# Optimization experiments

Measured on AMD Instinct MI355X. Metric: run time of the kernel, lower is better.

Reference implementation:

```python
import jax, jax.numpy as jnp
import numpy as np

N = 50000      # nodes
E = 800000     # edges (before self loops)
NF = 4         # node feature dim
EF = 4         # edge feature dim
EMB = 16       # joint embedding dim
HID = 64       # hidden dim
OUT = 128      # output dim
H = 4          # heads (layers 0,1); last layer has 1 head
NEG_SLOPE = 0.2


def setup_inputs() -> dict:
    key = jax.random.key(0)
    ks = jax.random.split(key, 20)
    in0 = NF + EMB  # 20

    def lin(k, o, i):
        return (jax.random.normal(k, (o, i), jnp.float32) * np.float32(1.0 / np.sqrt(i)))

    return {
        'x': jax.random.normal(ks[0], (N, NF), jnp.float32),
        'edge_index': jax.random.randint(ks[1], (2, E), 0, N, dtype=jnp.int32),
        'edge_attr': jax.random.normal(ks[2], (E, EF), jnp.float32),
        'joint_types': jax.random.randint(ks[3], (N,), 0, 17, dtype=jnp.int32),
        'emb_table': jax.random.normal(ks[4], (17, EMB), jnp.float32) * 0.1,
        'W0': lin(ks[5], H * HID, in0),
        'a_src0': jax.random.normal(ks[6], (H, HID), jnp.float32) * 0.1,
        'a_dst0': jax.random.normal(ks[7], (H, HID), jnp.float32) * 0.1,
        'We0': lin(ks[8], H, EF),
        'W1': lin(ks[9], H * HID, HID),
        'a_src1': jax.random.normal(ks[10], (H, HID), jnp.float32) * 0.1,
        'a_dst1': jax.random.normal(ks[11], (H, HID), jnp.float32) * 0.1,
        'We1': lin(ks[12], H, EF),
        'W2': lin(ks[13], 1 * OUT, HID),
        'a_src2': jax.random.normal(ks[14], (1, OUT), jnp.float32) * 0.1,
        'a_dst2': jax.random.normal(ks[15], (1, OUT), jnp.float32) * 0.1,
        'We2': lin(ks[16], 1, EF),
    }


def gat_layer(x, src, dst, eattr, W, a_src, a_dst, We, num_nodes):
    # x: [N, F_in]; W: [H*C, F_in]; a_src/a_dst: [H, C]; We: [H, EF]
    Hh, C = a_src.shape
    h = (x @ W.T).reshape(num_nodes, Hh, C)  # [N, H, C]
    # per-node attention scores, gathered per edge (same math as per-edge dot)
    s_i = jnp.einsum('nhc,hc->nh', h, a_src)  # applied to x_i = x[dst]
    s_j = jnp.einsum('nhc,hc->nh', h, a_dst)  # applied to x_j = x[src]
    alpha = s_i[dst] + s_j[src] + eattr @ We.T  # [Etot, H]
    alpha = jax.nn.leaky_relu(alpha, NEG_SLOPE)
    # faithful to torch.softmax(alpha, dim=0): GLOBAL softmax over all edges per head
    alpha = jax.nn.softmax(alpha, axis=0)
    msgs = h[src] * alpha[:, :, None]  # [Etot, H, C]
    out = jax.ops.segment_sum(msgs, dst, num_segments=num_nodes)  # aggr='add'
    return out.mean(axis=1)  # update(): mean over heads -> [N, C]


def reference(x, edge_index, edge_attr, joint_types, emb_table,
              W0, a_src0, a_dst0, We0,
              W1, a_src1, a_dst1, We1,
              W2, a_src2, a_dst2, We2):
    num_nodes = x.shape[0]
    # add self loops (edge_attr fill 0.0)
    loops = jnp.arange(num_nodes, dtype=edge_index.dtype)
    src = jnp.concatenate([edge_index[0], loops])
    dst = jnp.concatenate([edge_index[1], loops])
    eattr = jnp.concatenate([edge_attr, jnp.zeros((num_nodes, edge_attr.shape[1]), edge_attr.dtype)], axis=0)

    h = jnp.concatenate([x, emb_table[joint_types]], axis=-1)  # [N, 20]
    h = gat_layer(h, src, dst, eattr, W0, a_src0, a_dst0, We0, num_nodes)
    h = jax.nn.elu(h)  # dropout is identity in eval mode
    h = gat_layer(h, src, dst, eattr, W1, a_src1, a_dst1, We1, num_nodes)
    h = jax.nn.elu(h)
    h = gat_layer(h, src, dst, eattr, W2, a_src2, a_dst2, We2, num_nodes)
    return h  # [N, OUT]
```

## Files before the change

kernel.cpp:

```cpp
#include <hip/hip_runtime.h>
#include <math.h>

#define NN 50000
#define EE 800000
#define EEN (EE+NN)
#define STRIDE 64
#define NFEAT 4
#define EFEAT 4
#define EMBD 16
#define IN0 20
#define HIDD 64
#define OUTD 128

__device__ __forceinline__ unsigned short f2bf(float f){
  unsigned u = __float_as_uint(f);
  return (unsigned short)((u + 0x7FFFu + ((u>>16)&1u)) >> 16);
}
__device__ __forceinline__ float bfl(unsigned u){ return __uint_as_float(u<<16); }
__device__ __forceinline__ float bfh(unsigned u){ return __uint_as_float(u & 0xFFFF0000u); }

template<int V> struct ldt;
template<> struct ldt<4>{ using T = uint2; };
template<> struct ldt<2>{ using T = unsigned int; };

__global__ void k_init(int* fill){
  int i = blockIdx.x*blockDim.x + threadIdx.x;
  if (i < NN) fill[i]=0;
}

__global__ void k_scatter(const int* __restrict__ ei, int* fill,
                          int* __restrict__ col, int* __restrict__ epos){
  int idx = blockIdx.x*blockDim.x + threadIdx.x;
  if (idx < EE){
    int d = ei[EE+idx];
    int pos = atomicAdd(&fill[d],1);
    col[d*STRIDE + 1 + pos] = ei[idx];
    epos[idx] = d*STRIDE + 1 + pos;
  } else if (idx < EEN){
    int n = idx-EE;
    col[n*STRIDE] = n;
  }
}

template<int F_IN,int HH,int CC>
__device__ __forceinline__ void av_one(const float* W, const float* asrc,
                                       const float* adst, float* av, int tid){
  if (tid >= HH*F_IN) return;
  int h = tid / F_IN, f = tid % F_IN;
  float s1=0.f, s2=0.f;
  for (int c=0;c<CC;c++){
    float wv = W[(size_t)(h*CC+c)*F_IN+f];
    s1 += asrc[h*CC+c]*wv;
    s2 += adst[h*CC+c]*wv;
  }
  av[tid] = s1;
  av[HH*F_IN+tid] = s2;
}
__global__ void k_av3(const float* W0, const float* as0, const float* ad0, float* av0,
                      const float* W1, const float* as1, const float* ad1, float* av1,
                      const float* W2, const float* as2, const float* ad2, float* av2,
                      float* zred){
  int tid = threadIdx.x;
  if      (blockIdx.x==0){ av_one<IN0,4,64> (W0, as0, ad0, av0, tid); if (tid<24) zred[tid]=0.f; }
  else if (blockIdx.x==1) av_one<64,4,64>  (W1, as1, ad1, av1, tid);
  else                    av_one<64,1,128> (W2, as2, ad2, av2, tid);
}

template<int K,int NCOL,int HH,bool CONCAT>
__global__ __launch_bounds__(256)
void k_gemm(const float* __restrict__ xin, const int* __restrict__ jt,
            const float* __restrict__ emb, const float* __restrict__ W,
            const float* __restrict__ avp, unsigned short* __restrict__ hout,
            float* __restrict__ si, float* __restrict__ sj){
  constexpr int PITCH = 132;
  __shared__ float xT[K*PITCH];
  __shared__ float wT[K*PITCH];
  __shared__ float EMBL[CONCAT ? 17*EMBD : 1];
  int tid = threadIdx.x;
  int rbase = blockIdx.x*128, cbase = blockIdx.y*128;
  if (CONCAT){
    for (int i=tid; i<17*EMBD; i+=256) EMBL[i]=emb[i];
    __syncthreads();
    if (tid < 128){
      int row = tid;
      int gr = rbase+row; if (gr >= NN) gr = NN-1;
      float4 v = ((const float4*)xin)[gr];
      xT[0*PITCH+row]=v.x; xT[1*PITCH+row]=v.y;
      xT[2*PITCH+row]=v.z; xT[3*PITCH+row]=v.w;
      int j = jt[gr];
      #pragma unroll
      for (int k=0;k<EMBD;k++) xT[(NFEAT+k)*PITCH+row] = EMBL[j*EMBD+k];
    } else {
      int col = tid-128;
      const float4* wp = (const float4*)(W + (size_t)(cbase+col)*K);
      #pragma unroll
      for (int k4=0;k4<K/4;k4++){
        float4 v = wp[k4];
        wT[(4*k4+0)*PITCH+col]=v.x; wT[(4*k4+1)*PITCH+col]=v.y;
        wT[(4*k4+2)*PITCH+col]=v.z; wT[(4*k4+3)*PITCH+col]=v.w;
      }
    }
  } else {
    constexpr int K4 = K/4;
    for (int i=tid; i<128*K4; i+=256){
      int row = i/K4, k4 = i%K4;
      int gr = rbase+row; if (gr >= NN) gr = NN-1;
      float4 v = ((const float4*)xin)[(size_t)gr*K4 + k4];
      xT[(4*k4+0)*PITCH+row]=v.x; xT[(4*k4+1)*PITCH+row]=v.y;
      xT[(4*k4+2)*PITCH+row]=v.z; xT[(4*k4+3)*PITCH+row]=v.w;
    }
    for (int i=tid; i<128*K4; i+=256){
      int col = i/K4, k4 = i%K4;
      float4 v = ((const float4*)W)[(size_t)(cbase+col)*K4 + k4];
      wT[(4*k4+0)*PITCH+col]=v.x; wT[(4*k4+1)*PITCH+col]=v.y;
      wT[(4*k4+2)*PITCH+col]=v.z; wT[(4*k4+3)*PITCH+col]=v.w;
    }
  }
  __syncthreads();
  int lane = tid & 63, w = tid >> 6;
  int r0 = (w>>1)*64 + (lane&7)*8;
  int c0 = (w&1)*64 + (lane>>3)*8;
  float acc[8][8];
  #pragma unroll
  for (int i=0;i<8;i++)
    #pragma unroll
    for (int j=0;j<8;j++) acc[i][j]=0.f;
  #pragma unroll 4
  for (int k=0;k<K;k++){
    float a[8], b[8];
    *(float4*)&a[0] = *(const float4*)&xT[k*PITCH + r0];
    *(float4*)&a[4] = *(const float4*)&xT[k*PITCH + r0 + 4];
    *(float4*)&b[0] = *(const float4*)&wT[k*PITCH + c0];
    *(float4*)&b[4] = *(const float4*)&wT[k*PITCH + c0 + 4];
    #pragma unroll
    for (int i=0;i<8;i++)
      #pragma unroll
      for (int j=0;j<8;j++) acc[i][j] += a[i]*b[j];
  }
  if (blockIdx.y==0 && tid < 128){
    int row = tid, gr = rbase+row;
    if (gr < NN){
      #pragma unroll
      for (int h=0;h<HH;h++){
        float a=0.f, b=0.f;
        for (int k=0;k<K;k++){
          float xv = xT[k*PITCH+row];
          a += xv*avp[h*K+k];
          b += xv*avp[HH*K+h*K+k];
        }
        si[(size_t)gr*HH+h]=a;
        sj[(size_t)gr*HH+h]=b;
      }
    }
  }
  #pragma unroll
  for (int i=0;i<8;i++){
    int n = rbase + r0 + i;
    if (n < NN){
      uint4 o;
      o.x = (unsigned)f2bf(acc[i][0]) | ((unsigned)f2bf(acc[i][1])<<16);
      o.y = (unsigned)f2bf(acc[i][2]) | ((unsigned)f2bf(acc[i][3])<<16);
      o.z = (unsigned)f2bf(acc[i][4]) | ((unsigned)f2bf(acc[i][5])<<16);
      o.w = (unsigned)f2bf(acc[i][6]) | ((unsigned)f2bf(acc[i][7])<<16);
      *(uint4*)(hout + (size_t)n*NCOL + cbase + c0) = o;
    }
  }
}

template<int HH>
__global__ void k_edge(const int* __restrict__ ei, const float* __restrict__ eattr,
                       const float* __restrict__ We, const float* __restrict__ si,
                       const float* __restrict__ sj, const int* __restrict__ epos,
                       float* __restrict__ pp, float* __restrict__ zred){
  int idx = blockIdx.x*blockDim.x + threadIdx.x;
  float z[HH];
  #pragma unroll
  for (int h=0;h<HH;h++) z[h]=0.f;
  if (idx < EE){
    int s = ei[idx], d = ei[EE+idx];
    const float4 ea = ((const float4*)eattr)[idx];
    int pos = epos[idx];
    if (HH==4){
      float4 siv = ((const float4*)si)[d];
      float4 sjv = ((const float4*)sj)[s];
      float te[4] = {siv.x+sjv.x, siv.y+sjv.y, siv.z+sjv.z, siv.w+sjv.w};
      float pv[4];
      #pragma unroll
      for (int h=0;h<4;h++){
        float t = te[h] + ea.x*We[h*EFEAT+0] + ea.y*We[h*EFEAT+1]
                        + ea.z*We[h*EFEAT+2] + ea.w*We[h*EFEAT+3];
        t = (t>0.f)? t : 0.2f*t;
        float p = expf(t);
        z[h]=p; pv[h]=p;
      }
      ((float4*)pp)[pos] = make_float4(pv[0],pv[1],pv[2],pv[3]);
    } else {
      float t = si[d] + sj[s]
              + ea.x*We[0] + ea.y*We[1] + ea.z*We[2] + ea.w*We[3];
      t = (t>0.f)? t : 0.2f*t;
      float p = expf(t);
      z[0]=p;
      pp[pos] = p;
    }
  } else if (idx < EEN){
    int n = idx-EE;
    int pos = n*STRIDE;
    if (HH==4){
      float4 siv = ((const float4*)si)[n];
      float4 sjv = ((const float4*)sj)[n];
      float te[4] = {siv.x+sjv.x, siv.y+sjv.y, siv.z+sjv.z, siv.w+sjv.w};
      float pv[4];
      #pragma unroll
      for (int h=0;h<4;h++){
        float t = te[h];
        t = (t>0.f)? t : 0.2f*t;
        float p = expf(t);
        z[h]=p; pv[h]=p;
      }
      ((float4*)pp)[pos] = make_float4(pv[0],pv[1],pv[2],pv[3]);
    } else {
      float t = si[n]+sj[n];
      t = (t>0.f)? t : 0.2f*t;
      float p = expf(t);
      z[0]=p;
      pp[pos]=p;
    }
  }
  __shared__ float zs[4][HH];
  #pragma unroll
  for (int h=0;h<HH;h++){
    float v=z[h];
    #pragma unroll
    for (int off=32; off>0; off>>=1) v += __shfl_xor(v,off,64);
    if ((threadIdx.x&63)==0) zs[threadIdx.x>>6][h]=v;
  }
  __syncthreads();
  if (threadIdx.x < HH){
    float tot = zs[0][threadIdx.x]+zs[1][threadIdx.x]
              + zs[2][threadIdx.x]+zs[3][threadIdx.x];
    atomicAdd(&zred[threadIdx.x], tot);
  }
}

template<int HH,int CC,bool DO_ELU>
__global__ __launch_bounds__(256)
void k_agg(const unsigned short* __restrict__ hb, const float* __restrict__ pp,
           const float* __restrict__ zred, const int* __restrict__ fill,
           const int* __restrict__ col, float* __restrict__ outp){
  constexpr int HC = HH*CC;
  constexpr int V  = HC/64;
  using LT = typename ldt<V>::T;
  int wave = threadIdx.x>>6, lane = threadIdx.x&63;
  int n = blockIdx.x*4 + wave;
  int hd = (lane*V)/CC;
  float invZ = 1.0f/zred[hd];
  float acc[V];
  #pragma unroll
  for (int v=0;v<V;v++) acc[v]=0.f;
  auto mac = [&](float p, LT h){
    if constexpr (V==4){
      acc[0] += p*bfl(h.x); acc[1] += p*bfh(h.x);
      acc[2] += p*bfl(h.y); acc[3] += p*bfh(h.y);
    } else {
      acc[0] += p*bfl(h);   acc[1] += p*bfh(h);
    }
  };
  int beg = n*STRIDE, end = beg + 1 + fill[n];
  int i = beg;
  for (; i+8<=end; i+=8){
    int sr[8]; float p[8]; LT h[8];
    #pragma unroll
    for (int k=0;k<8;k++) sr[k]=col[i+k];
    #pragma unroll
    for (int k=0;k<8;k++)
      p[k] = (HH==4) ? pp[(size_t)(i+k)*4+hd] : pp[i+k];
    #pragma unroll
    for (int k=0;k<8;k++) h[k]=((const LT*)(hb + (size_t)sr[k]*HC))[lane];
    #pragma unroll
    for (int k=0;k<8;k++) mac(p[k], h[k]);
  }
  for (; i<end; i++){
    int sr = col[i];
    float p = (HH==4) ? pp[(size_t)i*4+hd] : pp[i];
    LT h = ((const LT*)(hb + (size_t)sr*HC))[lane];
    mac(p, h);
  }
  #pragma unroll
  for (int v=0;v<V;v++) acc[v] *= invZ;
  if (HH==4){
    #pragma unroll
    for (int off=16; off<64; off<<=1){
      #pragma unroll
      for (int v=0;v<V;v++) acc[v] += __shfl_xor(acc[v], off, 64);
    }
    if (lane < 16){
      float4 o;
      o.x=0.25f*acc[0]; o.y=0.25f*acc[1]; o.z=0.25f*acc[2]; o.w=0.25f*acc[3];
      if (DO_ELU){
        o.x = (o.x>0.f)? o.x : expm1f(o.x);
        o.y = (o.y>0.f)? o.y : expm1f(o.y);
        o.z = (o.z>0.f)? o.z : expm1f(o.z);
        o.w = (o.w>0.f)? o.w : expm1f(o.w);
      }
      ((float4*)outp)[(size_t)n*(CC/4)+lane] = o;
    }
  } else {
    float2 o; o.x=acc[0]; o.y=acc[1];
    if (DO_ELU){
      o.x = (o.x>0.f)? o.x : expm1f(o.x);
      o.y = (o.y>0.f)? o.y : expm1f(o.y);
    }
    ((float2*)outp)[(size_t)n*(CC/2)+lane] = o;
  }
}

extern "C" void kernel_launch(void* const* d_in, const int* in_sizes, int n_in,
                              void* d_out, int out_size, void* d_ws, size_t ws_size,
                              hipStream_t stream){
  const float* x    = (const float*)d_in[0];
  const int*   ei   = (const int*)d_in[1];
  const float* eatt = (const float*)d_in[2];
  const int*   jt   = (const int*)d_in[3];
  const float* emb  = (const float*)d_in[4];
  const float* W0   = (const float*)d_in[5];
  const float* as0  = (const float*)d_in[6];
  const float* ad0  = (const float*)d_in[7];
  const float* We0  = (const float*)d_in[8];
  const float* W1   = (const float*)d_in[9];
  const float* as1  = (const float*)d_in[10];
  const float* ad1  = (const float*)d_in[11];
  const float* We1  = (const float*)d_in[12];
  const float* W2   = (const float*)d_in[13];
  const float* as2  = (const float*)d_in[14];
  const float* ad2  = (const float*)d_in[15];
  const float* We2  = (const float*)d_in[16];
  float* out = (float*)d_out;

  char* p = (char*)d_ws;
  auto alloc = [&](size_t bytes)->char*{
    char* r = p; p += (bytes + 255) & ~(size_t)255; return r;
  };
  unsigned short* hbuf = (unsigned short*)alloc((size_t)NN*256*2);
  float* x1     = (float*)alloc((size_t)NN*64*4);
  float* x2     = (float*)alloc((size_t)NN*64*4);
  float* si     = (float*)alloc((size_t)NN*4*4);
  float* sj     = (float*)alloc((size_t)NN*4*4);
  float* pp     = (float*)alloc((size_t)NN*STRIDE*16);
  int*   fill   = (int*)alloc((size_t)NN*4);
  int*   col    = (int*)alloc((size_t)NN*STRIDE*4);
  int*   epos   = (int*)alloc((size_t)EE*4);
  float* av0    = (float*)alloc(512*4);
  float* av1    = (float*)alloc(512*4);
  float* av2    = (float*)alloc(512*4);
  float* zred   = (float*)alloc(3*8*4);

  k_init   <<<dim3((NN+255)/256),  256, 0, stream>>>(fill);
  k_scatter<<<dim3((EEN+255)/256), 256, 0, stream>>>(ei, fill, col, epos);
  k_av3    <<<dim3(3),             256, 0, stream>>>(W0,as0,ad0,av0, W1,as1,ad1,av1,
                                                     W2,as2,ad2,av2, zred);

  dim3 gg01((NN+127)/128, 2);
  dim3 gg2 ((NN+127)/128, 1);
  dim3 egrid((EEN+255)/256);
  dim3 agrid(NN/4);

  k_gemm<IN0,256,4,true> <<<gg01, 256, 0, stream>>>(x, jt, emb, W0, av0, hbuf, si, sj);
  k_edge<4>              <<<egrid,256, 0, stream>>>(ei, eatt, We0, si, sj, epos, pp, zred+0);
  k_agg<4,64,true>       <<<agrid,256, 0, stream>>>(hbuf, pp, zred+0, fill, col, x1);

  k_gemm<64,256,4,false> <<<gg01, 256, 0, stream>>>(x1, jt, emb, W1, av1, hbuf, si, sj);
  k_edge<4>              <<<egrid,256, 0, stream>>>(ei, eatt, We1, si, sj, epos, pp, zred+8);
  k_agg<4,64,true>       <<<agrid,256, 0, stream>>>(hbuf, pp, zred+8, fill, col, x2);

  k_gemm<64,128,1,false> <<<gg2,  256, 0, stream>>>(x2, jt, emb, W2, av2, hbuf, si, sj);
  k_edge<1>              <<<egrid,256, 0, stream>>>(ei, eatt, We2, si, sj, epos, pp, zred+16);
  k_agg<1,128,false>     <<<agrid,256, 0, stream>>>(hbuf, pp, zred+16, fill, col, out);
}
```

Before: 539.6 us.

## Reorder edge attributes into CSR slots and compute edge scores per destination node

The scatter pass now copies edge attributes into the padded CSR slot layout. The edge-score kernel then processes one destination node per wave, reading col and attributes contiguously and using the node's own si value. This removes the epos indirection, the random pp writes and the per-edge si gathers. In exchange the work per wave is capped at 64 lanes, so nodes with fewer edges leave lanes idle, and the padded attribute buffer is large.

```diff
diff --git a/kernel.cpp b/kernel.cpp
--- a/kernel.cpp
+++ b/kernel.cpp
@@ -28,14 +28,15 @@
   if (i < NN) fill[i]=0;
 }
 
-__global__ void k_scatter(const int* __restrict__ ei, int* fill,
-                          int* __restrict__ col, int* __restrict__ epos){
+__global__ void k_scatter(const int* __restrict__ ei, const float4* __restrict__ eattr,
+                          int* fill, int* __restrict__ col, float4* __restrict__ eacsr){
   int idx = blockIdx.x*blockDim.x + threadIdx.x;
   if (idx < EE){
     int d = ei[EE+idx];
     int pos = atomicAdd(&fill[d],1);
-    col[d*STRIDE + 1 + pos] = ei[idx];
-    epos[idx] = d*STRIDE + 1 + pos;
+    int slot = d*STRIDE + 1 + pos;
+    col[slot] = ei[idx];
+    eacsr[slot] = eattr[idx];
   } else if (idx < EEN){
     int n = idx-EE;
     col[n*STRIDE] = n;
@@ -168,20 +169,25 @@
 }
 
 template<int HH>
-__global__ void k_edge(const int* __restrict__ ei, const float* __restrict__ eattr,
-                       const float* __restrict__ We, const float* __restrict__ si,
-                       const float* __restrict__ sj, const int* __restrict__ epos,
-                       float* __restrict__ pp, float* __restrict__ zred){
-  int idx = blockIdx.x*blockDim.x + threadIdx.x;
+__global__ __launch_bounds__(256)
+void k_edge2(const int* __restrict__ col, const float4* __restrict__ eacsr,
+             const int* __restrict__ fill, const float* __restrict__ We,
+             const float* __restrict__ si, const float* __restrict__ sj,
+             float* __restrict__ pp, float* __restrict__ zred){
+  int wave = threadIdx.x>>6, lane = threadIdx.x&63;
+  int n = blockIdx.x*4 + wave;
+  int cnt = 1 + fill[n];
   float z[HH];
   #pragma unroll
   for (int h=0;h<HH;h++) z[h]=0.f;
-  if (idx < EE){
-    int s = ei[idx], d = ei[EE+idx];
-    const float4 ea = ((const float4*)eattr)[idx];
-    int pos = epos[idx];
+  if (lane < cnt){
+    int slot = n*STRIDE + lane;
+    int s = col[slot];
+    float4 ea;
+    if (lane==0){ ea = make_float4(0.f,0.f,0.f,0.f); }
+    else        { ea = eacsr[slot]; }
     if (HH==4){
-      float4 siv = ((const float4*)si)[d];
+      float4 siv = ((const float4*)si)[n];
       float4 sjv = ((const float4*)sj)[s];
       float te[4] = {siv.x+sjv.x, siv.y+sjv.y, siv.z+sjv.z, siv.w+sjv.w};
       float pv[4];
@@ -193,37 +199,14 @@
         float p = expf(t);
         z[h]=p; pv[h]=p;
       }
-      ((float4*)pp)[pos] = make_float4(pv[0],pv[1],pv[2],pv[3]);
+      ((float4*)pp)[slot] = make_float4(pv[0],pv[1],pv[2],pv[3]);
     } else {
-      float t = si[d] + sj[s]
+      float t = si[n] + sj[s]
               + ea.x*We[0] + ea.y*We[1] + ea.z*We[2] + ea.w*We[3];
       t = (t>0.f)? t : 0.2f*t;
       float p = expf(t);
       z[0]=p;
-      pp[pos] = p;
-    }
-  } else if (idx < EEN){
-    int n = idx-EE;
-    int pos = n*STRIDE;
-    if (HH==4){
-      float4 siv = ((const float4*)si)[n];
-      float4 sjv = ((const float4*)sj)[n];
-      float te[4] = {siv.x+sjv.x, siv.y+sjv.y, siv.z+sjv.z, siv.w+sjv.w};
-      float pv[4];
-      #pragma unroll
-      for (int h=0;h<4;h++){
-        float t = te[h];
-        t = (t>0.f)? t : 0.2f*t;
-        float p = expf(t);
-        z[h]=p; pv[h]=p;
-      }
-      ((float4*)pp)[pos] = make_float4(pv[0],pv[1],pv[2],pv[3]);
-    } else {
-      float t = si[n]+sj[n];
-      t = (t>0.f)? t : 0.2f*t;
-      float p = expf(t);
-      z[0]=p;
-      pp[pos]=p;
+      pp[slot] = p;
     }
   }
   __shared__ float zs[4][HH];
@@ -232,7 +215,7 @@
     float v=z[h];
     #pragma unroll
     for (int off=32; off>0; off>>=1) v += __shfl_xor(v,off,64);
-    if ((threadIdx.x&63)==0) zs[threadIdx.x>>6][h]=v;
+    if (lane==0) zs[wave][h]=v;
   }
   __syncthreads();
   if (threadIdx.x < HH){
@@ -348,31 +331,31 @@
   float* pp     = (float*)alloc((size_t)NN*STRIDE*16);
   int*   fill   = (int*)alloc((size_t)NN*4);
   int*   col    = (int*)alloc((size_t)NN*STRIDE*4);
-  int*   epos   = (int*)alloc((size_t)EE*4);
+  float4* eacsr = (float4*)alloc((size_t)NN*STRIDE*16);
   float* av0    = (float*)alloc(512*4);
   float* av1    = (float*)alloc(512*4);
   float* av2    = (float*)alloc(512*4);
   float* zred   = (float*)alloc(3*8*4);
 
   k_init   <<<dim3((NN+255)/256),  256, 0, stream>>>(fill);
-  k_scatter<<<dim3((EEN+255)/256), 256, 0, stream>>>(ei, fill, col, epos);
+  k_scatter<<<dim3((EEN+255)/256), 256, 0, stream>>>(ei, (const float4*)eatt,
+                                                     fill, col, eacsr);
   k_av3    <<<dim3(3),             256, 0, stream>>>(W0,as0,ad0,av0, W1,as1,ad1,av1,
                                                      W2,as2,ad2,av2, zred);
 
   dim3 gg01((NN+127)/128, 2);
   dim3 gg2 ((NN+127)/128, 1);
-  dim3 egrid((EEN+255)/256);
-  dim3 agrid(NN/4);
+  dim3 ngrid(NN/4);
 
   k_gemm<IN0,256,4,true> <<<gg01, 256, 0, stream>>>(x, jt, emb, W0, av0, hbuf, si, sj);
-  k_edge<4>              <<<egrid,256, 0, stream>>>(ei, eatt, We0, si, sj, epos, pp, zred+0);
-  k_agg<4,64,true>       <<<agrid,256, 0, stream>>>(hbuf, pp, zred+0, fill, col, x1);
+  k_edge2<4>             <<<ngrid,256, 0, stream>>>(col, eacsr, fill, We0, si, sj, pp, zred+0);
+  k_agg<4,64,true>       <<<ngrid,256, 0, stream>>>(hbuf, pp, zred+0, fill, col, x1);
 
   k_gemm<64,256,4,false> <<<gg01, 256, 0, stream>>>(x1, jt, emb, W1, av1, hbuf, si, sj);
-  k_edge<4>              <<<egrid,256, 0, stream>>>(ei, eatt, We1, si, sj, epos, pp, zred+8);
-  k_agg<4,64,true>       <<<agrid,256, 0, stream>>>(hbuf, pp, zred+8, fill, col, x2);
+  k_edge2<4>             <<<ngrid,256, 0, stream>>>(col, eacsr, fill, We1, si, sj, pp, zred+8);
+  k_agg<4,64,true>       <<<ngrid,256, 0, stream>>>(hbuf, pp, zred+8, fill, col, x2);
 
   k_gemm<64,128,1,false> <<<gg2,  256, 0, stream>>>(x2, jt, emb, W2, av2, hbuf, si, sj);
-  k_edge<1>              <<<egrid,256, 0, stream>>>(ei, eatt, We2, si, sj, epos, pp, zred+16);
-  k_agg<1,128,false>     <<<agrid,256, 0, stream>>>(hbuf, pp, zred+16, fill, col, out);
-}
+  k_edge2<1>             <<<ngrid,256, 0, stream>>>(col, eacsr, fill, We2, si, sj, pp, zred+16);
+  k_agg<1,128,false>     <<<ngrid,256, 0, stream>>>(hbuf, pp, zred+16, fill, col, out);
+}
```

Measured after the change: 881.7 us. 63.4% more time.
